# Optimization experiments

Measured on AMD Instinct MI355X. Metric: run time of the kernel, lower is better.

The kernel has to match this reference:

```python
import jax, jax.numpy as jnp
import numpy as np

NUM_BINS = 256


def _equalize_channel(chan):
    # chan: (P,) int32 pixel values in [0, 255]. PIL/torchvision-style equalize.
    hist = jnp.zeros(NUM_BINS, jnp.float32).at[chan].add(1.0)
    total = hist.sum()
    # value of the last nonzero histogram bin (excluded from step computation)
    nz = hist > 0
    last_idx = (NUM_BINS - 1) - jnp.argmax(nz[::-1])
    last = hist[last_idx]
    step = jnp.floor((total - last) / 255.0)
    cum = jnpp_cumsum = jnp.cumsum(hist)
    lut = jnp.floor((cum + jnp.floor(step / 2.0)) / jnp.maximum(step, 1.0))
    # shift right by one (pad a leading 0, drop last) and clamp to [0,255]
    lut = jnp.clip(jnp.concatenate([jnp.zeros(1, jnp.float32), lut[:-1]]), 0.0, 255.0)
    ident = jnp.arange(NUM_BINS, dtype=jnp.float32)
    lut = jnp.where(step == 0, ident, lut)  # step==0 -> identity mapping
    return lut[chan]


def _equalize(x):
    # x: (N, C, H, W) float, pixel values -> uint8 semantics
    N, C, H, W = x.shape
    xi = jnp.clip(x, 0, 255).astype(jnp.int32).reshape(N * C, H * W)
    out = jax.vmap(_equalize_channel)(xi)  # (N*C, H*W) float32
    return out.reshape(N, C, H, W).astype(x.dtype)


def setup_inputs() -> dict:
    key = jax.random.key(0)
    x = jax.random.uniform(key, (64, 3, 512, 512), dtype=jnp.float32) * 255.0
    magnitude = 5
    return {"x": x, "magnitude": magnitude}


def reference(x, magnitude):
    # magnitude is unused in the original forward (Equalize ignores it)
    return _equalize(x)
```

## Files before the change

kernel.cpp:

```cpp
#include <hip/hip_runtime.h>

#define NBINS 256
#define NCHAN 192
#define TPB 1024
#define VEC_PER_CHAN 65536
#define NCOPY 32

typedef float f4 __attribute__((ext_vector_type(4)));

__global__ __launch_bounds__(TPB) void equalize_fused(const float* __restrict__ x,
                                                      float* __restrict__ out) {
    __shared__ int   lh[NBINS * NCOPY];
    __shared__ float slut[NBINS * NCOPY];
    __shared__ int   scan[NBINS];
    __shared__ int   s_last_idx, s_last;

    const int chan = blockIdx.x;
    const int tid  = threadIdx.x;
    const int cp   = (tid & 63) >> 1;

    for (int i = tid; i < NBINS * NCOPY; i += TPB) lh[i] = 0;
    if (tid == 0) s_last_idx = 0;
    __syncthreads();

    const size_t base = (size_t)chan * VEC_PER_CHAN;
    const f4* bx = (const f4*)x + base;

    #pragma unroll 4
    for (int i = tid; i < VEC_PER_CHAN; i += TPB) {
        f4 v = bx[i];
        int a = (int)fminf(fmaxf(v.x, 0.f), 255.f);
        int b = (int)fminf(fmaxf(v.y, 0.f), 255.f);
        int c = (int)fminf(fmaxf(v.z, 0.f), 255.f);
        int d = (int)fminf(fmaxf(v.w, 0.f), 255.f);
        atomicAdd(&lh[(a << 5) + cp], 1);
        atomicAdd(&lh[(b << 5) + cp], 1);
        atomicAdd(&lh[(c << 5) + cp], 1);
        atomicAdd(&lh[(d << 5) + cp], 1);
    }
    __syncthreads();

    int h = 0;
    if (tid < NBINS) {
        #pragma unroll
        for (int k = 0; k < NCOPY; ++k) h += lh[(tid << 5) + ((tid + k) & 31)];
        scan[tid] = h;
    }
    __syncthreads();
    if (tid < NBINS && h > 0) atomicMax(&s_last_idx, tid);

    for (int off = 1; off < NBINS; off <<= 1) {
        int t = 0;
        if (tid >= off && tid < NBINS) t = scan[tid - off];
        __syncthreads();
        if (tid < NBINS) scan[tid] += t;
        __syncthreads();
    }
    if (tid == s_last_idx) s_last = h;
    __syncthreads();

    const int total = scan[NBINS - 1];
    const int step  = (total - s_last) / 255;

    if (tid < NBINS) {
        float lutv;
        if (step == 0)      lutv = (float)tid;
        else if (tid == 0)  lutv = 0.f;
        else {
            int l = (scan[tid - 1] + (step >> 1)) / step;
            lutv = (float)(l < 255 ? l : 255);
        }
        #pragma unroll
        for (int k = 0; k < NCOPY; ++k) slut[(tid << 5) + ((tid + k) & 31)] = lutv;
    }
    __syncthreads();

    f4* bo = (f4*)out + base;
    #pragma unroll 4
    for (int i = tid; i < VEC_PER_CHAN; i += TPB) {
        f4 v = bx[i];
        int a = (int)fminf(fmaxf(v.x, 0.f), 255.f);
        int b = (int)fminf(fmaxf(v.y, 0.f), 255.f);
        int c = (int)fminf(fmaxf(v.z, 0.f), 255.f);
        int d = (int)fminf(fmaxf(v.w, 0.f), 255.f);
        f4 o;
        o.x = slut[(a << 5) + cp];
        o.y = slut[(b << 5) + cp];
        o.z = slut[(c << 5) + cp];
        o.w = slut[(d << 5) + cp];
        __builtin_nontemporal_store(o, &bo[i]);
    }
}

extern "C" void kernel_launch(void* const* d_in, const int* in_sizes, int n_in,
                              void* d_out, int out_size, void* d_ws, size_t ws_size,
                              hipStream_t stream) {
    const float* x = (const float*)d_in[0];
    float* out = (float*)d_out;
    (void)d_ws; (void)ws_size;

    equalize_fused<<<NCHAN, TPB, 0, stream>>>(x, out);
}
```

Before: 365.5 us.

## Split each channel across four blocks with redundant histograms and XCD-aware mapping

Launches four 256-thread blocks per channel instead of one 1024-thread block. Each block redundantly builds the full channel histogram and LUT, then applies the LUT to only its quarter of the pixels. Block IDs are remapped so the four blocks of a channel land on the same XCD and can share L2 for the repeated reads, and the LUT now reuses the histogram's shared memory to halve LDS use. The aim is more blocks per CU and more concurrency, paid for by reading each channel's input four times during the histogram phase.

```diff
diff --git a/kernel.cpp b/kernel.cpp
--- a/kernel.cpp
+++ b/kernel.cpp
@@ -1,59 +1,60 @@
 #include <hip/hip_runtime.h>
+
 
 #define NBINS 256
 #define NCHAN 192
-#define TPB 1024
-#define VEC_PER_CHAN 65536
+#define BPC 4
+#define TPB 256
 #define NCOPY 32
+#define F4_PER_CHAN 65536
+#define F4_PER_STRIP 16384
 
 typedef float f4 __attribute__((ext_vector_type(4)));
 
-__global__ __launch_bounds__(TPB) void equalize_fused(const float* __restrict__ x,
+__device__ __forceinline__ int clamp_u8(float v) {
+    return (int)fminf(fmaxf(v, 0.f), 255.f);
+}
+
+__global__ __launch_bounds__(TPB) void eq_hist4_apply(const float* __restrict__ x,
                                                       float* __restrict__ out) {
-    __shared__ int   lh[NBINS * NCOPY];
-    __shared__ float slut[NBINS * NCOPY];
-    __shared__ int   scan[NBINS];
-    __shared__ int   s_last_idx, s_last;
+    __shared__ int lh[NBINS * NCOPY];
+    __shared__ int scan[NBINS];
+    __shared__ int s_last_idx, s_last;
 
-    const int chan = blockIdx.x;
-    const int tid  = threadIdx.x;
-    const int cp   = (tid & 63) >> 1;
+    const int tid = threadIdx.x;
+    const int cp  = (tid & 63) >> 1;
+
+    const int bid  = blockIdx.x;
+    const int xcd  = bid & 7;
+    const int slot = bid >> 3;
+    const int chan = (slot >> 2) * 8 + xcd;
+    const int blk  = slot & 3;
 
     for (int i = tid; i < NBINS * NCOPY; i += TPB) lh[i] = 0;
     if (tid == 0) s_last_idx = 0;
     __syncthreads();
 
-    const size_t base = (size_t)chan * VEC_PER_CHAN;
-    const f4* bx = (const f4*)x + base;
-
-    #pragma unroll 4
-    for (int i = tid; i < VEC_PER_CHAN; i += TPB) {
-        f4 v = bx[i];
-        int a = (int)fminf(fmaxf(v.x, 0.f), 255.f);
-        int b = (int)fminf(fmaxf(v.y, 0.f), 255.f);
-        int c = (int)fminf(fmaxf(v.z, 0.f), 255.f);
-        int d = (int)fminf(fmaxf(v.w, 0.f), 255.f);
-        atomicAdd(&lh[(a << 5) + cp], 1);
-        atomicAdd(&lh[(b << 5) + cp], 1);
-        atomicAdd(&lh[(c << 5) + cp], 1);
-        atomicAdd(&lh[(d << 5) + cp], 1);
+    const f4* cx = (const f4*)x + (size_t)chan * F4_PER_CHAN;
+    for (int i = tid; i < F4_PER_CHAN; i += TPB) {
+        f4 v = cx[i];
+        atomicAdd(&lh[(clamp_u8(v.x) << 5) + cp], 1);
+        atomicAdd(&lh[(clamp_u8(v.y) << 5) + cp], 1);
+        atomicAdd(&lh[(clamp_u8(v.z) << 5) + cp], 1);
+        atomicAdd(&lh[(clamp_u8(v.w) << 5) + cp], 1);
     }
     __syncthreads();
 
     int h = 0;
-    if (tid < NBINS) {
-        #pragma unroll
-        for (int k = 0; k < NCOPY; ++k) h += lh[(tid << 5) + ((tid + k) & 31)];
-        scan[tid] = h;
-    }
+    #pragma unroll
+    for (int k = 0; k < NCOPY; ++k) h += lh[(tid << 5) + ((tid + k) & 31)];
+    scan[tid] = h;
     __syncthreads();
-    if (tid < NBINS && h > 0) atomicMax(&s_last_idx, tid);
+    if (h > 0) atomicMax(&s_last_idx, tid);
 
     for (int off = 1; off < NBINS; off <<= 1) {
-        int t = 0;
-        if (tid >= off && tid < NBINS) t = scan[tid - off];
+        int t = (tid >= off) ? scan[tid - off] : 0;
         __syncthreads();
-        if (tid < NBINS) scan[tid] += t;
+        scan[tid] += t;
         __syncthreads();
     }
     if (tid == s_last_idx) s_last = h;
@@ -62,32 +63,29 @@
     const int total = scan[NBINS - 1];
     const int step  = (total - s_last) / 255;
 
-    if (tid < NBINS) {
-        float lutv;
-        if (step == 0)      lutv = (float)tid;
-        else if (tid == 0)  lutv = 0.f;
-        else {
-            int l = (scan[tid - 1] + (step >> 1)) / step;
-            lutv = (float)(l < 255 ? l : 255);
-        }
-        #pragma unroll
-        for (int k = 0; k < NCOPY; ++k) slut[(tid << 5) + ((tid + k) & 31)] = lutv;
+    float lutv;
+    if (step == 0)      lutv = (float)tid;
+    else if (tid == 0)  lutv = 0.f;
+    else {
+        int l = (scan[tid - 1] + (step >> 1)) / step;
+        lutv = (float)(l < 255 ? l : 255);
     }
+    float* slut = (float*)lh;
+    #pragma unroll
+    for (int k = 0; k < NCOPY; ++k) slut[(tid << 5) + ((tid + k) & 31)] = lutv;
     __syncthreads();
 
-    f4* bo = (f4*)out + base;
-    #pragma unroll 4
-    for (int i = tid; i < VEC_PER_CHAN; i += TPB) {
+    const size_t sb = (size_t)chan * F4_PER_CHAN + (size_t)blk * F4_PER_STRIP;
+    const f4* bx = (const f4*)x + sb;
+    f4* bo = (f4*)out + sb;
+
+    for (int i = tid; i < F4_PER_STRIP; i += TPB) {
         f4 v = bx[i];
-        int a = (int)fminf(fmaxf(v.x, 0.f), 255.f);
-        int b = (int)fminf(fmaxf(v.y, 0.f), 255.f);
-        int c = (int)fminf(fmaxf(v.z, 0.f), 255.f);
-        int d = (int)fminf(fmaxf(v.w, 0.f), 255.f);
         f4 o;
-        o.x = slut[(a << 5) + cp];
-        o.y = slut[(b << 5) + cp];
-        o.z = slut[(c << 5) + cp];
-        o.w = slut[(d << 5) + cp];
+        o.x = slut[(clamp_u8(v.x) << 5) + cp];
+        o.y = slut[(clamp_u8(v.y) << 5) + cp];
+        o.z = slut[(clamp_u8(v.z) << 5) + cp];
+        o.w = slut[(clamp_u8(v.w) << 5) + cp];
         __builtin_nontemporal_store(o, &bo[i]);
     }
 }
@@ -99,5 +97,5 @@
     float* out = (float*)d_out;
     (void)d_ws; (void)ws_size;
 
-    equalize_fused<<<NCHAN, TPB, 0, stream>>>(x, out);
+    eq_hist4_apply<<<NCHAN * BPC, TPB, 0, stream>>>(x, out);
 }
```

New measurement: 458.6 us. +25.5%, slower.
